# Kernel optimization log

Measured on AMD Instinct MI355X. Metric: run time of the kernel, lower is better.

Reference implementation:

```python
import jax, jax.numpy as jnp
import numpy as np

NUM_USERS = 100000
NUM_ITEMS = 50000
NUM_NODES = NUM_USERS + NUM_ITEMS
NUM_LAYERS = 4
DIM_H = 64
NUM_EDGES = 1200000


def setup_inputs() -> dict:
    key = jax.random.key(0)
    k1, k2, k3 = jax.random.split(key, 3)
    user_emb = jax.random.normal(k1, (NUM_USERS, DIM_H), dtype=jnp.float32) * 0.01
    item_emb = jax.random.normal(k2, (NUM_ITEMS, DIM_H), dtype=jnp.float32) * 0.01
    edge_index = jax.random.randint(k3, (2, NUM_EDGES), 0, NUM_NODES, dtype=jnp.int64)
    return {"user_emb": user_emb, "item_emb": item_emb, "edge_index": edge_index}


def _lightgcn_final(user_emb, item_emb, edge_index):
    row, col = edge_index[0], edge_index[1]  # src, dst
    # symmetric gcn_norm without self-loops (PyG LGConv default)
    deg = jax.ops.segment_sum(jnp.ones((edge_index.shape[1],), dtype=user_emb.dtype),
                              col, num_segments=NUM_NODES)
    dinv = jnp.where(deg > 0, jax.lax.rsqrt(deg), 0.0)
    norm = dinv[row] * dinv[col]  # [E]

    emb = jnp.concatenate([user_emb, item_emb], axis=0)  # [N, d]
    acc = emb  # running sum over layer embeddings (incl. layer 0)
    for _ in range(NUM_LAYERS):
        # out[dst] += norm * emb[src]  (normalized adjacency SpMM)
        emb = jax.ops.segment_sum(norm[:, None] * emb[row], col, num_segments=NUM_NODES)
        acc = acc + emb
    # faithful to source: mean over (L+1) embs, then an extra 1/(L+1) factor
    emb_final = acc / ((NUM_LAYERS + 1) ** 2)
    return emb_final


def reference(user_emb, item_emb, edge_index):
    emb_final = _lightgcn_final(user_emb, item_emb, edge_index)
    return emb_final[:NUM_USERS], emb_final[NUM_USERS:]
```

## Files before the change

kernel.cpp:

```cpp
#include <hip/hip_runtime.h>


#define DIMH 64
#define BLK 256
#define BSHIFT 9
#define BNODES 512
#define EB 8192

typedef float    f4  __attribute__((ext_vector_type(4)));
typedef _Float16 h4  __attribute__((ext_vector_type(4)));

__global__ void k_init(const float* __restrict__ uemb, const float* __restrict__ iemb,
                       _Float16* __restrict__ embA, float* __restrict__ acc,
                       int* __restrict__ bucketCnt, long uElems, long totalElems) {
    long t = (long)blockIdx.x * BLK + threadIdx.x;
    if (t < 1024) bucketCnt[t] = 0;
    long base = t * 4;
    if (base >= totalElems) return;
    f4 v = (base < uElems) ? *(const f4*)(uemb + base)
                           : *(const f4*)(iemb + (base - uElems));
    *(h4*)(embA + base) = __builtin_convertvector(v, h4);
    *(f4*)(acc + base) = v * (1.0f / 25.0f);
}

__global__ void k_binhist(const int* __restrict__ col, int* __restrict__ bucketCnt,
                          long E) {
    __shared__ int h[BNODES];
    for (int i = threadIdx.x; i < BNODES; i += BLK) h[i] = 0;
    __syncthreads();
    const long stride = (long)gridDim.x * BLK;
    for (long e = (long)blockIdx.x * BLK + threadIdx.x; e < E; e += stride)
        atomicAdd(&h[col[e] >> BSHIFT], 1);
    __syncthreads();
    for (int i = threadIdx.x; i < BNODES; i += BLK)
        if (h[i]) atomicAdd(&bucketCnt[i], h[i]);
}

__global__ void k_binscan(const int* __restrict__ bucketCnt, int* __restrict__ bucketPtr,
                          int* __restrict__ bucketCur, int NB, int E,
                          int* __restrict__ rowptrN) {
    __shared__ int lds[BLK];
    int t = threadIdx.x;
    int v0 = (2 * t < NB) ? bucketCnt[2 * t] : 0;
    int v1 = (2 * t + 1 < NB) ? bucketCnt[2 * t + 1] : 0;
    lds[t] = v0 + v1;
    __syncthreads();
    for (int off = 1; off < BLK; off <<= 1) {
        int mine = lds[t];
        int add = (t >= off) ? lds[t - off] : 0;
        __syncthreads();
        lds[t] = mine + add;
        __syncthreads();
    }
    int excl = (t > 0) ? lds[t - 1] : 0;
    if (2 * t < NB)     { bucketPtr[2 * t] = excl;          bucketCur[2 * t] = excl; }
    if (2 * t + 1 < NB) { bucketPtr[2 * t + 1] = excl + v0; bucketCur[2 * t + 1] = excl + v0; }
    if (t == 0) { bucketPtr[NB] = E; *rowptrN = E; }
}

__global__ void k_binscatter(const int* __restrict__ row, const int* __restrict__ col,
                             int* __restrict__ bucketCur, int2* __restrict__ staging,
                             long E) {
    __shared__ int h[BNODES];
    __shared__ int gb[BNODES];
    __shared__ int lc[BNODES];
    const long e0 = (long)blockIdx.x * EB;
    const int n = (int)((E - e0 < EB) ? (E - e0) : EB);
    for (int i = threadIdx.x; i < BNODES; i += BLK) h[i] = 0;
    __syncthreads();
    for (int i = threadIdx.x; i < n; i += BLK)
        atomicAdd(&h[col[e0 + i] >> BSHIFT], 1);
    __syncthreads();
    for (int b = threadIdx.x; b < BNODES; b += BLK) {
        int c = h[b];
        gb[b] = c ? atomicAdd(&bucketCur[b], c) : 0;
        lc[b] = 0;
    }
    __syncthreads();
    for (int i = threadIdx.x; i < n; i += BLK) {
        int c = col[e0 + i];
        int r = row[e0 + i];
        int b = c >> BSHIFT;
        int pos = gb[b] + atomicAdd(&lc[b], 1);
        staging[pos] = make_int2(r, c);
    }
}

__global__ void k_bucket(const int2* __restrict__ staging, const int* __restrict__ bucketPtr,
                         int* __restrict__ edges, int* __restrict__ rowptr,
                         float* __restrict__ dinv, _Float16* __restrict__ embA, long N) {
    __shared__ int cnt[BNODES];
    __shared__ int cur[BNODES];
    __shared__ float dnv[BNODES];
    __shared__ int lds[BLK];
    const int b = blockIdx.x;
    const long lo = (long)b << BSHIFT;
    const int R = (int)(((N - lo) < BNODES) ? (N - lo) : BNODES);
    const int beg = bucketPtr[b];
    const int end = bucketPtr[b + 1];
    const int t = threadIdx.x;

    for (int i = t; i < BNODES; i += BLK) cnt[i] = 0;
    __syncthreads();
    for (int e = beg + t; e < end; e += BLK)
        atomicAdd(&cnt[staging[e].y - (int)lo], 1);
    __syncthreads();

    int v0 = cnt[2 * t];
    int v1 = cnt[2 * t + 1];
    lds[t] = v0 + v1;
    __syncthreads();
    for (int off = 1; off < BLK; off <<= 1) {
        int mine = lds[t];
        int add = (t >= off) ? lds[t - off] : 0;
        __syncthreads();
        lds[t] = mine + add;
        __syncthreads();
    }
    int excl = (t > 0) ? lds[t - 1] : 0;
    int e0 = beg + excl;
    int e1 = e0 + v0;
    cur[2 * t] = e0;
    cur[2 * t + 1] = e1;
    dnv[2 * t] = (v0 > 0) ? rsqrtf((float)v0) : 0.0f;
    dnv[2 * t + 1] = (v1 > 0) ? rsqrtf((float)v1) : 0.0f;
    if (2 * t < R) {
        rowptr[lo + 2 * t] = e0;
        dinv[lo + 2 * t] = dnv[2 * t];
    }
    if (2 * t + 1 < R) {
        rowptr[lo + 2 * t + 1] = e1;
        dinv[lo + 2 * t + 1] = dnv[2 * t + 1];
    }
    __syncthreads();

    for (int e = beg + t; e < end; e += BLK) {
        int2 p = staging[e];
        int pos = atomicAdd(&cur[p.y - (int)lo], 1);
        edges[pos] = p.x;
    }

    for (int i = t; i < R * 16; i += BLK) {
        int nloc = i >> 4;
        int q = i & 15;
        float d = dnv[nloc];
        h4* p = (h4*)(embA + (lo + nloc) * DIMH) + q;
        f4 v = __builtin_convertvector(*p, f4);
        *p = __builtin_convertvector(v * d, h4);
    }
}

__global__ void __launch_bounds__(BLK)
k_gather(const _Float16* __restrict__ cur, _Float16* __restrict__ nxt,
         float* __restrict__ acc, const float* __restrict__ dinv,
         const int* __restrict__ rowptr, const int* __restrict__ edges,
         long N, int storeNxt) {
    long g = (long)blockIdx.x * BLK + threadIdx.x;
    if (g >= N * 16) return;
    long node = g >> 4;
    int q = (int)(g & 15);

    int beg = rowptr[node];
    int end = rowptr[node + 1];

    f4 s = {0.f, 0.f, 0.f, 0.f};
    f4 t2 = {0.f, 0.f, 0.f, 0.f};
    for (int base = beg; base < end; base += 16) {
        int me = base + q;
        int psrc = (me < end) ? edges[me] : 0;
        int n = end - base;
        if (n > 16) n = 16;
        int j = 0;
        for (; j + 4 <= n; j += 4) {
            int a0 = __shfl(psrc, j + 0, 16);
            int a1 = __shfl(psrc, j + 1, 16);
            int a2 = __shfl(psrc, j + 2, 16);
            int a3 = __shfl(psrc, j + 3, 16);
            h4 v0 = ((const h4*)(cur + (long)a0 * DIMH))[q];
            h4 v1 = ((const h4*)(cur + (long)a1 * DIMH))[q];
            h4 v2 = ((const h4*)(cur + (long)a2 * DIMH))[q];
            h4 v3 = ((const h4*)(cur + (long)a3 * DIMH))[q];
            s  += __builtin_convertvector(v0, f4);
            t2 += __builtin_convertvector(v1, f4);
            s  += __builtin_convertvector(v2, f4);
            t2 += __builtin_convertvector(v3, f4);
        }
        for (; j < n; ++j) {
            int a = __shfl(psrc, j, 16);
            h4 v = ((const h4*)(cur + (long)a * DIMH))[q];
            s += __builtin_convertvector(v, f4);
        }
    }
    s += t2;

    float d = dinv[node];
    f4 e = s * d;

    long off = node * DIMH + q * 4;
    f4 a = *(const f4*)(acc + off);
    *(f4*)(acc + off) = a + e * (1.0f / 25.0f);
    if (storeNxt)
        *(h4*)(nxt + off) = __builtin_convertvector(e * d, h4);
}

extern "C" void kernel_launch(void* const* d_in, const int* in_sizes, int n_in,
                              void* d_out, int out_size, void* d_ws, size_t ws_size,
                              hipStream_t stream) {
    const float* uemb = (const float*)d_in[0];
    const float* iemb = (const float*)d_in[1];
    const int*   edge = (const int*)d_in[2];

    const long uElems = in_sizes[0];
    const long iElems = in_sizes[1];
    const long E      = in_sizes[2] / 2;
    const long total  = uElems + iElems;
    const long N      = total / DIMH;

    const int* row = edge;
    const int* col = edge + E;

    float* acc = (float*)d_out;

    const int NB = (int)((N + BNODES - 1) >> BSHIFT);

    const long Npad = (N + 63) & ~63L;
    const long Epad = (E + 63) & ~63L;
    int*      rowptr    = (int*)d_ws;
    float*    dinv      = (float*)(rowptr + Npad + 64);
    int*      edges     = (int*)(dinv + Npad);
    int*      bucketCnt = edges + Epad;
    int*      bucketPtr = bucketCnt + 1024;
    int*      bucketCur = bucketPtr + 1024;
    _Float16* embA      = (_Float16*)(bucketCur + 1024);
    _Float16* embB      = embA + total;
    int2*     staging   = (int2*)embB;

    const long total4 = total / 4;
    const int gInit = (int)((total4 + BLK - 1) / BLK);
    k_init<<<gInit, BLK, 0, stream>>>(uemb, iemb, embA, acc, bucketCnt, uElems, total);
    k_binhist<<<512, BLK, 0, stream>>>(col, bucketCnt, E);
    k_binscan<<<1, BLK, 0, stream>>>(bucketCnt, bucketPtr, bucketCur, NB, (int)E,
                                     rowptr + N);
    k_binscatter<<<(int)((E + EB - 1) / EB), BLK, 0, stream>>>(row, col, bucketCur,
                                                               staging, E);
    k_bucket<<<NB, BLK, 0, stream>>>(staging, bucketPtr, edges, rowptr, dinv, embA, N);

    _Float16* cur = embA;
    _Float16* nxt = embB;
    const int gGather = (int)((N * 16 + BLK - 1) / BLK);
    for (int l = 0; l < 4; ++l) {
        k_gather<<<gGather, BLK, 0, stream>>>(cur, nxt, acc, dinv, rowptr, edges, N,
                                              (l < 3) ? 1 : 0);
        _Float16* t = cur; cur = nxt; nxt = t;
    }
}
```

Measured before the change: 307.7 us.

## Defer per-layer fp32 accumulation into one final combine kernel over stored fp16 layers

Each propagation layer now writes only its pre-scaled fp16 output to its own buffer and no longer reads and rewrites the fp32 accumulator. A new k_final kernel reads the four stored layer outputs, undoes the extra dinv scaling with 1/d, and adds them to the accumulator once. This is meant to cut the repeated fp32 read-modify-write traffic on the accumulator in every layer. In exchange it needs three more fp16 embedding buffers in workspace, adds one launch, and rebuilds each layer's value by dividing out d, which adds some fp16 rounding.

Result: faster. 294.9 us (-4.2%).

```diff
diff --git a/kernel.cpp b/kernel.cpp
--- a/kernel.cpp
+++ b/kernel.cpp
@@ -152,9 +152,8 @@
 
 __global__ void __launch_bounds__(BLK)
 k_gather(const _Float16* __restrict__ cur, _Float16* __restrict__ nxt,
-         float* __restrict__ acc, const float* __restrict__ dinv,
-         const int* __restrict__ rowptr, const int* __restrict__ edges,
-         long N, int storeNxt) {
+         const float* __restrict__ dinv,
+         const int* __restrict__ rowptr, const int* __restrict__ edges, long N) {
     long g = (long)blockIdx.x * BLK + threadIdx.x;
     if (g >= N * 16) return;
     long node = g >> 4;
@@ -194,13 +193,26 @@
     s += t2;
 
     float d = dinv[node];
-    f4 e = s * d;
-
+    ((h4*)(nxt + node * DIMH))[q] = __builtin_convertvector(s * (d * d), h4);
+}
+
+__global__ void __launch_bounds__(BLK)
+k_final(const _Float16* __restrict__ z1, const _Float16* __restrict__ z2,
+        const _Float16* __restrict__ z3, const _Float16* __restrict__ z4,
+        const float* __restrict__ dinv, float* __restrict__ acc, long N) {
+    long g = (long)blockIdx.x * BLK + threadIdx.x;
+    if (g >= N * 16) return;
+    long node = g >> 4;
+    int q = (int)(g & 15);
+    float d = dinv[node];
+    float f = (d > 0.f) ? (1.0f / d) * (1.0f / 25.0f) : 0.f;
     long off = node * DIMH + q * 4;
+    f4 zs = __builtin_convertvector(*(const h4*)(z1 + off), f4)
+          + __builtin_convertvector(*(const h4*)(z2 + off), f4)
+          + __builtin_convertvector(*(const h4*)(z3 + off), f4)
+          + __builtin_convertvector(*(const h4*)(z4 + off), f4);
     f4 a = *(const f4*)(acc + off);
-    *(f4*)(acc + off) = a + e * (1.0f / 25.0f);
-    if (storeNxt)
-        *(h4*)(nxt + off) = __builtin_convertvector(e * d, h4);
+    *(f4*)(acc + off) = a + zs * f;
 }
 
 extern "C" void kernel_launch(void* const* d_in, const int* in_sizes, int n_in,
@@ -232,8 +244,11 @@
     int*      bucketPtr = bucketCnt + 1024;
     int*      bucketCur = bucketPtr + 1024;
     _Float16* embA      = (_Float16*)(bucketCur + 1024);
-    _Float16* embB      = embA + total;
-    int2*     staging   = (int2*)embB;
+    _Float16* zb0       = embA + total;
+    _Float16* zb1       = zb0 + total;
+    _Float16* zb2       = zb1 + total;
+    _Float16* zb3       = zb2 + total;
+    int2*     staging   = (int2*)zb0;
 
     const long total4 = total / 4;
     const int gInit = (int)((total4 + BLK - 1) / BLK);
@@ -245,12 +260,9 @@
                                                                staging, E);
     k_bucket<<<NB, BLK, 0, stream>>>(staging, bucketPtr, edges, rowptr, dinv, embA, N);
 
-    _Float16* cur = embA;
-    _Float16* nxt = embB;
     const int gGather = (int)((N * 16 + BLK - 1) / BLK);
-    for (int l = 0; l < 4; ++l) {
-        k_gather<<<gGather, BLK, 0, stream>>>(cur, nxt, acc, dinv, rowptr, edges, N,
-                                              (l < 3) ? 1 : 0);
-        _Float16* t = cur; cur = nxt; nxt = t;
-    }
-}
+    _Float16* zs[5] = {embA, zb0, zb1, zb2, zb3};
+    for (int l = 0; l < 4; ++l)
+        k_gather<<<gGather, BLK, 0, stream>>>(zs[l], zs[l + 1], dinv, rowptr, edges, N);
+    k_final<<<gGather, BLK, 0, stream>>>(zb0, zb1, zb2, zb3, dinv, acc, N);
+}
```
